# Performance work log

Hardware: AMD Instinct MI355X
Metric: run time of the kernel (lower is better)

## Reference

```python
import jax, jax.numpy as jnp
import numpy as np

B, S, D, H = 2, 2048, 1024, 16
DK = D // H

def setup_inputs() -> dict:
    key = jax.random.key(0)
    ks = jax.random.split(key, 12)
    scale = 1.0 / np.sqrt(D)
    return {
        "q": jax.random.normal(ks[0], (B, S, D), jnp.float32),
        "k": jax.random.normal(ks[1], (B, S, D), jnp.float32),
        "v": jax.random.normal(ks[2], (B, S, D), jnp.float32),
        "mask": jax.random.randint(ks[3], (B, 1, S, S), 0, 2, jnp.int32),
        "w_q": jax.random.normal(ks[4], (D, D), jnp.float32) * scale,
        "b_q": jnp.zeros((D,), jnp.float32),
        "w_k": jax.random.normal(ks[5], (D, D), jnp.float32) * scale,
        "b_k": jnp.zeros((D,), jnp.float32),
        "w_v": jax.random.normal(ks[6], (D, D), jnp.float32) * scale,
        "b_v": jnp.zeros((D,), jnp.float32),
        "w_o": jax.random.normal(ks[7], (D, D), jnp.float32) * scale,
        "b_o": jnp.zeros((D,), jnp.float32),
    }

def reference(q, k, v, mask, w_q, b_q, w_k, b_k, w_v, b_v, w_o, b_o):
    # projections (nn.Linear: x @ W^T + b)
    Q = q @ w_q.T + b_q  # [B,S,D]
    K = k @ w_k.T + b_k
    V = v @ w_v.T + b_v
    # split heads -> [B,H,S,DK]
    Q = Q.reshape(B, S, H, DK).transpose(0, 2, 1, 3)
    K = K.reshape(B, S, H, DK).transpose(0, 2, 1, 3)
    V = V.reshape(B, S, H, DK).transpose(0, 2, 1, 3)
    scores = jnp.einsum("bhqd,bhkd->bhqk", Q, K) / jnp.sqrt(jnp.float32(DK))
    scores = jnp.where(mask == 0, jnp.float32(-1e9), scores)
    attn = jax.nn.softmax(scores, axis=-1)  # dropout p=0 -> identity
    x = jnp.einsum("bhqk,bhkd->bhqd", attn, V)
    x = x.transpose(0, 2, 1, 3).reshape(B, S, D)
    return x @ w_o.T + b_o
```

## Files before the change

### kernel.cpp

```cpp
#include <hip/hip_runtime.h>
#include <hip/hip_bf16.h>
#include <cstdint>
#include <cstddef>

typedef short bf16x8 __attribute__((ext_vector_type(8)));
typedef short bf16x4v __attribute__((ext_vector_type(4)));
typedef float f32x4 __attribute__((ext_vector_type(4)));
typedef unsigned int uint32x2 __attribute__((ext_vector_type(2)));
typedef __hip_bfloat16 bf16;

constexpr int Bb = 2, Ss = 2048, Dd = 1024, Hh = 16, DKk = 64;

__device__ __forceinline__ void async_lds16(void* lds, const void* g) {
  __builtin_amdgcn_global_load_lds(
      (const __attribute__((address_space(1))) void*)g,
      (__attribute__((address_space(3))) void*)lds, 16, 0, 0);
}

__device__ __forceinline__ float bf2f(bf16 x) { return __bfloat162float(x); }
__device__ __forceinline__ short f2bf(float x) {
  bf16 h = __float2bfloat16(x);
  return *(short*)&h;
}
__device__ __forceinline__ short f2bf_fast(float x) {
  return (short)((__float_as_uint(x) + 0x8000u) >> 16);
}
__device__ __forceinline__ float bfs2f(short s) {
  return __uint_as_float(((uint32_t)(uint16_t)s) << 16);
}
__device__ __forceinline__ uint32_t cvtpk_bf16(float lo, float hi) {
  uint32_t r;
  asm("v_cvt_pk_bf16_f32 %0, %1, %2" : "=v"(r) : "v"(lo), "v"(hi));
  return r;
}
__device__ __forceinline__ uint32x2 pl32swap(uint32_t d, uint32_t s) {
  return __builtin_amdgcn_permlane32_swap(d, s, false, false);
}
__device__ __forceinline__ uint32x2 pl16swap(uint32_t d, uint32_t s) {
  return __builtin_amdgcn_permlane16_swap(d, s, false, false);
}

struct CvtArgs {
  const float* src[12];
  short* dst[12];
  int n[12];
  int count;
};

__global__ __launch_bounds__(256)
void cvt_all(CvtArgs a, const int* __restrict__ mask, uint32_t* __restrict__ bits)
{
  const int t = blockIdx.y;
  if (t == 11) {
    const int stride = 1024 * 256;
    int i = blockIdx.x * 256 + threadIdx.x;
#pragma unroll 4
    for (int it = 0; it < 32; ++it, i += stride) {
      const unsigned long long bal = __ballot(mask[i] != 0);
      if ((threadIdx.x & 63) == 0)
        *(unsigned long long*)(bits + (i >> 5)) = bal;
    }
    return;
  }
  if (t >= a.count) return;
  const float* s = a.src[t];
  short* d = a.dst[t];
  const int n = a.n[t];
  const int stride = gridDim.x * blockDim.x * 4;
  for (int i = (blockIdx.x * blockDim.x + threadIdx.x) * 4; i < n; i += stride) {
    const float4 v = *(const float4*)(s + i);
    bf16x4v o;
    o[0] = f2bf(v.x); o[1] = f2bf(v.y); o[2] = f2bf(v.z); o[3] = f2bf(v.w);
    *(bf16x4v*)(d + i) = o;
  }
}

__global__ __launch_bounds__(256, 3)
void gemm_bt(const bf16* __restrict__ A0, const bf16* __restrict__ A1, const bf16* __restrict__ A2,
             const bf16* __restrict__ W0, const bf16* __restrict__ W1, const bf16* __restrict__ W2,
             const bf16* __restrict__ b0, const bf16* __restrict__ b1, const bf16* __restrict__ b2,
             void* __restrict__ O0, void* __restrict__ O1, void* __restrict__ O2,
             float scale0, int vtrans)
{
  extern __shared__ char smem[];
  const int mt  = blockIdx.x;
  const int by  = blockIdx.y;
  const int mat = by >> 3;
  const int nt  = by & 7;
  const bf16* A    = (mat == 0) ? A0 : (mat == 1) ? A1 : A2;
  const bf16* W    = (mat == 0) ? W0 : (mat == 1) ? W1 : W2;
  const bf16* bias = (mat == 0) ? b0 : (mat == 1) ? b1 : b2;
  void*       Out  = (mat == 0) ? O0 : (mat == 1) ? O1 : O2;
  const float scale = (mat == 0) ? scale0 : 1.0f;

  const int tid  = threadIdx.x;
  const int w    = tid >> 6;
  const int lane = tid & 63;
  const int quad = lane >> 4;
  const int l16  = lane & 15;
  const int wm   = (w & 1) * 64;
  const int wn   = (w >> 1) * 64;

  const int srow = lane >> 3;
  const int sseg = (lane & 7) ^ srow;

  const char* Abytes = (const char*)A;
  const char* Wbytes = (const char*)W;

  f32x4 acc[4][4];
#pragma unroll
  for (int i = 0; i < 4; ++i)
#pragma unroll
    for (int j = 0; j < 4; ++j) acc[i][j] = f32x4{0.f, 0.f, 0.f, 0.f};

  for (int kt = 0; kt < 16; ++kt) {
    __syncthreads();
#pragma unroll
    for (int c = 0; c < 4; ++c) {
      const int r0 = w * 32 + c * 8;
      async_lds16(smem + r0 * 128,
                  Abytes + (size_t)(mt * 128 + r0 + srow) * 2048 + kt * 128 + sseg * 16);
      async_lds16(smem + 16384 + r0 * 128,
                  Wbytes + (size_t)(nt * 128 + r0 + srow) * 2048 + kt * 128 + sseg * 16);
    }
    __syncthreads();
#pragma unroll
    for (int s = 0; s < 2; ++s) {
      bf16x8 af[4], bfg[4];
#pragma unroll
      for (int mb = 0; mb < 4; ++mb) {
        const int row = wm + mb * 16 + l16;
        af[mb] = *(const bf16x8*)(smem + row * 128 + (((4 * s + quad) ^ (row & 7)) * 16));
      }
#pragma unroll
      for (int nb = 0; nb < 4; ++nb) {
        const int row = wn + nb * 16 + l16;
        bfg[nb] = *(const bf16x8*)(smem + 16384 + row * 128 + (((4 * s + quad) ^ (row & 7)) * 16));
      }
#pragma unroll
      for (int mb = 0; mb < 4; ++mb)
#pragma unroll
        for (int nb = 0; nb < 4; ++nb)
          acc[mb][nb] = __builtin_amdgcn_mfma_f32_16x16x32_bf16(af[mb], bfg[nb], acc[mb][nb], 0, 0, 0);
    }
  }

  if (vtrans && mat == 2) {
    __syncthreads();
#pragma unroll
    for (int nb = 0; nb < 4; ++nb) {
      const int dk = wn + nb * 16 + l16;
      const float bv = bf2f(bias[nt * 128 + dk]);
#pragma unroll
      for (int mb = 0; mb < 4; ++mb) {
        const int s0 = wm + mb * 16 + quad * 4;
        bf16x4v pk;
#pragma unroll
        for (int r = 0; r < 4; ++r) pk[r] = f2bf_fast(acc[mb][nb][r] + bv);
        *(bf16x4v*)(smem + dk * 256 + (((s0 >> 3) ^ (dk & 15)) * 16) + (s0 & 7) * 2) = pk;
      }
    }
    __syncthreads();
    const int bidx  = (mt * 128) >> 11;
    const int sbase = (mt * 128) & 2047;
#pragma unroll
    for (int i = 0; i < 8; ++i) {
      const int dk  = i * 16 + (tid >> 4);
      const int seg = tid & 15;
      bf16x8 vrow = *(const bf16x8*)(smem + dk * 256 + ((seg ^ (dk & 15)) * 16));
      *(bf16x8*)((bf16*)Out + (size_t)bidx * 2097152 + (size_t)(nt * 128 + dk) * 2048
                 + sbase + seg * 8) = vrow;
    }
  } else {
#pragma unroll
    for (int nb = 0; nb < 4; ++nb) {
      const int col = nt * 128 + wn + nb * 16 + l16;
      const float bv = bf2f(bias[col]);
#pragma unroll
      for (int mb = 0; mb < 4; ++mb) {
#pragma unroll
        for (int r = 0; r < 4; ++r) {
          const int row = mt * 128 + wm + mb * 16 + quad * 4 + r;
          short s = f2bf_fast((acc[mb][nb][r] + bv) * scale);
          ((short*)Out)[(size_t)row * 1024 + col] = s;
        }
      }
    }
  }
}

__global__ __launch_bounds__(256, 4)
void gemm_out(const bf16* __restrict__ A, const bf16* __restrict__ W,
              const bf16* __restrict__ bias, float* __restrict__ Out)
{
  __shared__ char smem[16384];
  const int mt = blockIdx.x;
  const int nt = blockIdx.y;
  const int tid = threadIdx.x, w = tid >> 6, lane = tid & 63;
  const int quad = lane >> 4, l16 = lane & 15;
  const int wm = (w & 1) * 32, wn = (w >> 1) * 32;
  const int srow = lane >> 3;
  const int sseg = (lane & 7) ^ (srow & 7);

  const char* Abytes = (const char*)A;
  const char* Wbytes = (const char*)W;

  f32x4 acc[2][2];
#pragma unroll
  for (int i = 0; i < 2; ++i)
#pragma unroll
    for (int j = 0; j < 2; ++j) acc[i][j] = f32x4{0.f, 0.f, 0.f, 0.f};

  for (int kt = 0; kt < 16; ++kt) {
    __syncthreads();
#pragma unroll
    for (int c = 0; c < 2; ++c) {
      const int r0 = c * 32 + w * 8;
      async_lds16(smem + c * 4096 + w * 1024,
                  Abytes + (size_t)(mt * 64 + r0 + srow) * 2048 + kt * 128 + sseg * 16);
      async_lds16(smem + 8192 + c * 4096 + w * 1024,
                  Wbytes + (size_t)(nt * 64 + r0 + srow) * 2048 + kt * 128 + sseg * 16);
    }
    __syncthreads();
#pragma unroll
    for (int s = 0; s < 2; ++s) {
      bf16x8 af[2], bfg[2];
#pragma unroll
      for (int mb = 0; mb < 2; ++mb) {
        const int row = wm + mb * 16 + l16;
        af[mb] = *(const bf16x8*)(smem + row * 128 + (((4 * s + quad) ^ (row & 7)) * 16));
      }
#pragma unroll
      for (int nb = 0; nb < 2; ++nb) {
        const int row = wn + nb * 16 + l16;
        bfg[nb] = *(const bf16x8*)(smem + 8192 + row * 128 + (((4 * s + quad) ^ (row & 7)) * 16));
      }
#pragma unroll
      for (int mb = 0; mb < 2; ++mb)
#pragma unroll
        for (int nb = 0; nb < 2; ++nb)
          acc[mb][nb] = __builtin_amdgcn_mfma_f32_16x16x32_bf16(af[mb], bfg[nb], acc[mb][nb], 0, 0, 0);
    }
  }

#pragma unroll
  for (int nb = 0; nb < 2; ++nb) {
    const int col = nt * 64 + wn + nb * 16 + l16;
    const float bv = bf2f(bias[col]);
#pragma unroll
    for (int mb = 0; mb < 2; ++mb) {
#pragma unroll
      for (int r = 0; r < 4; ++r) {
        const int row = mt * 64 + wm + mb * 16 + quad * 4 + r;
        Out[(size_t)row * 1024 + col] = acc[mb][nb][r] + bv;
      }
    }
  }
}

__device__ __forceinline__ void stage_kv(char* KbB, char* VtB,
    const bf16* __restrict__ Kp, const bf16* __restrict__ VpT,
    size_t headoff, size_t vbase, int kb, int w, int lane)
{
#pragma unroll
  for (int c = 0; c < 4; ++c) {
    const int rowK = c * 32 + w * 8 + (lane >> 3);
    const int segK = (lane & 7) ^ (rowK & 7);
    async_lds16(KbB + c * 4096 + w * 1024,
                Kp + headoff + (size_t)(kb + rowK) * Dd + segK * 8);
    const int rowV = c * 16 + w * 4 + (lane >> 4);
    const int segV = (lane & 15) ^ (rowV & 15);
    async_lds16(VtB + c * 4096 + w * 1024,
                VpT + vbase + (size_t)rowV * 2048 + kb + segV * 8);
  }
}

__global__ __launch_bounds__(256, 2)
void attn(const bf16* __restrict__ Qp, const bf16* __restrict__ Kp,
          const bf16* __restrict__ VpT, const uint32_t* __restrict__ mbits,
          bf16* __restrict__ Opart, float* __restrict__ Lpart)
{
  __shared__ char smem[65536];

  const int tile  = blockIdx.x;
  const int split = blockIdx.y;
  const int qt = tile & 15, h = (tile >> 4) & 15, b = tile >> 8;
  const int tid = threadIdx.x, w = tid >> 6, lane = tid & 63;
  const int quad = lane >> 4, l16 = lane & 15;
  const int qb = qt * 128;
  const size_t headoff = (size_t)b * (Ss * Dd) + h * DKk;
  const size_t vbase = (size_t)b * 2097152 + (size_t)h * 131072;

  const int kc0 = split * 8;
  const int kc1 = kc0 + 8;

  bf16x8 qf[2][2];
#pragma unroll
  for (int set = 0; set < 2; ++set)
#pragma unroll
    for (int s2 = 0; s2 < 2; ++s2) {
      const int row = qb + w * 32 + set * 16 + l16;
      qf[set][s2] = *(const bf16x8*)(Qp + headoff + (size_t)row * Dd + s2 * 32 + quad * 8);
    }

  bf16x8 onesv;
#pragma unroll
  for (int j = 0; j < 8; ++j) onesv[j] = (short)0x3F80;

  f32x4 o[2][4];
  f32x4 oL[2];
#pragma unroll
  for (int set = 0; set < 2; ++set) {
    oL[set] = f32x4{0.f, 0.f, 0.f, 0.f};
#pragma unroll
    for (int nbk = 0; nbk < 4; ++nbk) o[set][nbk] = f32x4{0.f, 0.f, 0.f, 0.f};
  }

  const uint32_t* mrow0 = mbits + (size_t)(b * Ss + qb + w * 32 + l16) * 64;
  const uint32_t* mrow1 = mrow0 + 16 * 64;

  char* KbC = smem;
  char* VtC = smem + 16384;
  char* KbN = smem + 32768;
  char* VtN = smem + 49152;

  uint4 mc0v = *(const uint4*)(mrow0 + kc0 * 4);
  uint4 mc1v = *(const uint4*)(mrow1 + kc0 * 4);
  stage_kv(KbC, VtC, Kp, VpT, headoff, vbase, kc0 * 128, w, lane);

  for (int kc = kc0; kc < kc1; ++kc) {
    uint4 mn0v = mc0v, mn1v = mc1v;
    if (kc + 1 < kc1) {
      mn0v = *(const uint4*)(mrow0 + (kc + 1) * 4);
      mn1v = *(const uint4*)(mrow1 + (kc + 1) * 4);
      stage_kv(KbN, VtN, Kp, VpT, headoff, vbase, (kc + 1) * 128, w, lane);
      asm volatile("s_waitcnt vmcnt(8)" ::: "memory");
    } else {
      asm volatile("s_waitcnt vmcnt(0)" ::: "memory");
    }
    __builtin_amdgcn_s_barrier();
    __builtin_amdgcn_sched_barrier(0);

    const uint32_t mc0a[4] = {mc0v.x, mc0v.y, mc0v.z, mc0v.w};
    const uint32_t mc1a[4] = {mc1v.x, mc1v.y, mc1v.z, mc1v.w};

#pragma unroll
    for (int sl = 0; sl < 4; ++sl) {
      f32x4 sc[2][2];
#pragma unroll
      for (int set = 0; set < 2; ++set)
#pragma unroll
        for (int nbh = 0; nbh < 2; ++nbh) sc[set][nbh] = f32x4{0.f, 0.f, 0.f, 0.f};
      __builtin_amdgcn_s_setprio(1);
#pragma unroll
      for (int s2 = 0; s2 < 2; ++s2)
#pragma unroll
        for (int nbh = 0; nbh < 2; ++nbh) {
          const int row = (sl * 2 + nbh) * 16 + l16;
          bf16x8 kf = *(const bf16x8*)(KbC + row * 128 + (((s2 * 4 + quad) ^ (row & 7)) * 16));
          sc[0][nbh] = __builtin_amdgcn_mfma_f32_16x16x32_bf16(kf, qf[0][s2], sc[0][nbh], 0, 0, 0);
          sc[1][nbh] = __builtin_amdgcn_mfma_f32_16x16x32_bf16(kf, qf[1][s2], sc[1][nbh], 0, 0, 0);
        }
      __builtin_amdgcn_s_setprio(0);

      bf16x8 pf[2];
#pragma unroll
      for (int set = 0; set < 2; ++set) {
        const uint32_t mword = (set == 0) ? mc0a[sl] : mc1a[sl];
        uint32_t pk[2][2];
#pragma unroll
        for (int nbh = 0; nbh < 2; ++nbh) {
          const uint32_t nib = (mword >> (nbh * 16 + quad * 4)) & 0xFu;
          const float e0 = __builtin_amdgcn_exp2f(sc[set][nbh][0]);
          const float e1 = __builtin_amdgcn_exp2f(sc[set][nbh][1]);
          const float e2 = __builtin_amdgcn_exp2f(sc[set][nbh][2]);
          const float e3 = __builtin_amdgcn_exp2f(sc[set][nbh][3]);
          const float p0 = (nib & 1u) ? e0 : 0.f;
          const float p1 = (nib & 2u) ? e1 : 0.f;
          const float p2 = (nib & 4u) ? e2 : 0.f;
          const float p3 = (nib & 8u) ? e3 : 0.f;
          pk[nbh][0] = cvtpk_bf16(p0, p1);
          pk[nbh][1] = cvtpk_bf16(p2, p3);
        }
        const uint32x2 r0 = pl32swap(pk[0][0], pk[1][0]);
        const uint32x2 r1 = pl32swap(pk[0][1], pk[1][1]);
        const uint32x2 t0 = pl16swap(r0.x, r0.y);
        const uint32x2 t1 = pl16swap(r1.x, r1.y);
        union { uint32_t u[4]; bf16x8 v; } U;
        U.u[0] = t0.x; U.u[1] = t1.x; U.u[2] = t0.y; U.u[3] = t1.y;
        pf[set] = U.v;
      }

      __builtin_amdgcn_s_setprio(1);
      oL[0] = __builtin_amdgcn_mfma_f32_16x16x32_bf16(pf[0], onesv, oL[0], 0, 0, 0);
      oL[1] = __builtin_amdgcn_mfma_f32_16x16x32_bf16(pf[1], onesv, oL[1], 0, 0, 0);
#pragma unroll
      for (int nbk = 0; nbk < 4; ++nbk) {
        const int row = nbk * 16 + l16;
        bf16x8 vf = *(const bf16x8*)(VtC + row * 256 + (((sl * 4 + quad) ^ (row & 15)) * 16));
        o[0][nbk] = __builtin_amdgcn_mfma_f32_16x16x32_bf16(pf[0], vf, o[0][nbk], 0, 0, 0);
        o[1][nbk] = __builtin_amdgcn_mfma_f32_16x16x32_bf16(pf[1], vf, o[1][nbk], 0, 0, 0);
      }
      __builtin_amdgcn_s_setprio(0);
    }

    asm volatile("" ::: "memory");
    __builtin_amdgcn_s_barrier();

    char* tp;
    tp = KbC; KbC = KbN; KbN = tp;
    tp = VtC; VtC = VtN; VtN = tp;
    mc0v = mn0v; mc1v = mn1v;
  }

#pragma unroll
  for (int set = 0; set < 2; ++set) {
    const int rbase = tile * 128 + w * 32 + set * 16;
#pragma unroll
    for (int r = 0; r < 4; ++r) {
      const int rglob = rbase + quad * 4 + r;
#pragma unroll
      for (int nbk = 0; nbk < 4; ++nbk) {
        short s = f2bf_fast(o[set][nbk][r]);
        ((short*)Opart)[((size_t)split * 65536 + rglob) * 64 + nbk * 16 + l16] = s;
      }
    }
    if (l16 == 0) {
#pragma unroll
      for (int r = 0; r < 4; ++r)
        Lpart[(size_t)split * 65536 + rbase + quad * 4 + r] = oL[set][r];
    }
  }
}

__global__ __launch_bounds__(256)
void combine(const bf16* __restrict__ Opart, const float* __restrict__ Lpart,
             bf16* __restrict__ Xa)
{
  const int t = threadIdx.x;
  const int row = blockIdx.x * 32 + (t >> 3);
  const int dkc = (t & 7) * 8;
  const float L = Lpart[row] + Lpart[65536 + row];
  const float inv = 1.0f / L;
  const bf16x8 O0 = *(const bf16x8*)(Opart + (size_t)row * 64 + dkc);
  const bf16x8 O1 = *(const bf16x8*)(Opart + ((size_t)65536 + row) * 64 + dkc);
  bf16x8 res;
#pragma unroll
  for (int j = 0; j < 8; ++j)
    res[j] = f2bf_fast((bfs2f(O0[j]) + bfs2f(O1[j])) * inv);
  const int tile = row >> 7, qlocal = row & 127;
  const int b = tile >> 8, h = (tile >> 4) & 15, q = (tile & 15) * 128 + qlocal;
  *(bf16x8*)(Xa + (size_t)(b * 2048 + q) * 1024 + h * 64 + dkc) = res;
}

extern "C" void kernel_launch(void* const* d_in, const int* in_sizes, int n_in,
                              void* d_out, int out_size, void* d_ws, size_t ws_size,
                              hipStream_t stream)
{
  const float* q  = (const float*)d_in[0];
  const float* k  = (const float*)d_in[1];
  const float* v  = (const float*)d_in[2];
  const int*   mk = (const int*)d_in[3];
  const float* wq = (const float*)d_in[4];
  const float* bq = (const float*)d_in[5];
  const float* wk = (const float*)d_in[6];
  const float* bk = (const float*)d_in[7];
  const float* wv = (const float*)d_in[8];
  const float* bv = (const float*)d_in[9];
  const float* wo = (const float*)d_in[10];
  const float* bo = (const float*)d_in[11];
  float* out = (float*)d_out;

  char* ws = (char*)d_ws;
  bf16* qb_  = (bf16*)(ws + ((size_t)0  << 20));
  bf16* kb_  = (bf16*)(ws + ((size_t)8  << 20));
  bf16* vb_  = (bf16*)(ws + ((size_t)16 << 20));
  bf16* Qp   = (bf16*)(ws + ((size_t)24 << 20));
  bf16* Kp   = (bf16*)(ws + ((size_t)32 << 20));
  bf16* VpT  = (bf16*)(ws + ((size_t)40 << 20));
  bf16* wqb  = (bf16*)(ws + ((size_t)48 << 20));
  bf16* wkb  = (bf16*)(ws + ((size_t)50 << 20));
  bf16* wvb  = (bf16*)(ws + ((size_t)52 << 20));
  bf16* wob  = (bf16*)(ws + ((size_t)54 << 20));
  bf16* bqb  = (bf16*)(ws + ((size_t)56 << 20));
  bf16* bkb  = (bf16*)(ws + ((size_t)56 << 20) + 2048);
  bf16* bvb  = (bf16*)(ws + ((size_t)56 << 20) + 4096);
  bf16* bob  = (bf16*)(ws + ((size_t)56 << 20) + 6144);
  uint32_t* mbits = (uint32_t*)(ws + ((size_t)56 << 20) + 65536);
  bf16*  Opart = (bf16*)(ws + ((size_t)0 << 20));
  float* Lpart = (float*)(ws + ((size_t)48 << 20));
  bf16*  Xa    = (bf16*)(ws + ((size_t)24 << 20));

  const int NA = Bb * Ss * Dd;
  const int NW = Dd * Dd;

  CvtArgs ca;
  ca.src[0] = q;  ca.dst[0] = (short*)qb_; ca.n[0] = NA;
  ca.src[1] = k;  ca.dst[1] = (short*)kb_; ca.n[1] = NA;
  ca.src[2] = v;  ca.dst[2] = (short*)vb_; ca.n[2] = NA;
  ca.src[3] = wq; ca.dst[3] = (short*)wqb; ca.n[3] = NW;
  ca.src[4] = wk; ca.dst[4] = (short*)wkb; ca.n[4] = NW;
  ca.src[5] = wv; ca.dst[5] = (short*)wvb; ca.n[5] = NW;
  ca.src[6] = wo; ca.dst[6] = (short*)wob; ca.n[6] = NW;
  ca.src[7] = bq; ca.dst[7] = (short*)bqb; ca.n[7] = Dd;
  ca.src[8] = bk; ca.dst[8] = (short*)bkb; ca.n[8] = Dd;
  ca.src[9] = bv; ca.dst[9] = (short*)bvb; ca.n[9] = Dd;
  ca.src[10] = bo; ca.dst[10] = (short*)bob; ca.n[10] = Dd;
  ca.src[11] = bo; ca.dst[11] = (short*)bob; ca.n[11] = 0;
  ca.count = 11;

  dim3 blk(256);
  cvt_all<<<dim3(1024, 12), blk, 0, stream>>>(ca, mk, mbits);

  gemm_bt<<<dim3(32, 24), blk, 32768, stream>>>(qb_, kb_, vb_, wqb, wkb, wvb,
                                                bqb, bkb, bvb,
                                                (void*)Qp, (void*)Kp, (void*)VpT,
                                                0.125f * 1.44269504088896340736f, 1);
  attn<<<dim3(512, 2), blk, 0, stream>>>(Qp, Kp, VpT, mbits, Opart, Lpart);
  combine<<<dim3(2048), blk, 0, stream>>>(Opart, Lpart, Xa);
  gemm_out<<<dim3(64, 16), blk, 0, stream>>>(Xa, wob, bob, out);
}
```

Measured before the change: 254.9 us.

## Drop K/V double buffering to halve LDS and raise occupancy

Replaces the double-buffered K/V LDS staging with a single 32 KB buffer that is loaded and then synchronized each iteration. The launch-bounds hint is raised to allow four blocks per CU. The aim is to hide memory latency through more resident waves rather than explicit software prefetch. In exchange, loads no longer overlap compute within a block. The tighter register budget from the higher occupancy hint may cause spills.

```diff
diff --git a/kernel.cpp b/kernel.cpp
--- a/kernel.cpp
+++ b/kernel.cpp
@@ -275,12 +275,14 @@
   }
 }
 
-__global__ __launch_bounds__(256, 2)
+__global__ __launch_bounds__(256, 4)
 void attn(const bf16* __restrict__ Qp, const bf16* __restrict__ Kp,
           const bf16* __restrict__ VpT, const uint32_t* __restrict__ mbits,
           bf16* __restrict__ Opart, float* __restrict__ Lpart)
 {
-  __shared__ char smem[65536];
+  __shared__ char smem[32768];
+  char* Kb = smem;
+  char* Vt = smem + 16384;
 
   const int tile  = blockIdx.x;
   const int split = blockIdx.y;
@@ -319,30 +321,16 @@
   const uint32_t* mrow0 = mbits + (size_t)(b * Ss + qb + w * 32 + l16) * 64;
   const uint32_t* mrow1 = mrow0 + 16 * 64;
 
-  char* KbC = smem;
-  char* VtC = smem + 16384;
-  char* KbN = smem + 32768;
-  char* VtN = smem + 49152;
-
-  uint4 mc0v = *(const uint4*)(mrow0 + kc0 * 4);
-  uint4 mc1v = *(const uint4*)(mrow1 + kc0 * 4);
-  stage_kv(KbC, VtC, Kp, VpT, headoff, vbase, kc0 * 128, w, lane);
-
   for (int kc = kc0; kc < kc1; ++kc) {
-    uint4 mn0v = mc0v, mn1v = mc1v;
-    if (kc + 1 < kc1) {
-      mn0v = *(const uint4*)(mrow0 + (kc + 1) * 4);
-      mn1v = *(const uint4*)(mrow1 + (kc + 1) * 4);
-      stage_kv(KbN, VtN, Kp, VpT, headoff, vbase, (kc + 1) * 128, w, lane);
-      asm volatile("s_waitcnt vmcnt(8)" ::: "memory");
-    } else {
-      asm volatile("s_waitcnt vmcnt(0)" ::: "memory");
-    }
-    __builtin_amdgcn_s_barrier();
-    __builtin_amdgcn_sched_barrier(0);
-
-    const uint32_t mc0a[4] = {mc0v.x, mc0v.y, mc0v.z, mc0v.w};
-    const uint32_t mc1a[4] = {mc1v.x, mc1v.y, mc1v.z, mc1v.w};
+    const int kb = kc * 128;
+    const uint4 mwv0 = *(const uint4*)(mrow0 + kc * 4);
+    const uint4 mwv1 = *(const uint4*)(mrow1 + kc * 4);
+    __syncthreads();
+    stage_kv(Kb, Vt, Kp, VpT, headoff, vbase, kb, w, lane);
+    __syncthreads();
+
+    const uint32_t mw0[4] = {mwv0.x, mwv0.y, mwv0.z, mwv0.w};
+    const uint32_t mw1[4] = {mwv1.x, mwv1.y, mwv1.z, mwv1.w};
 
 #pragma unroll
     for (int sl = 0; sl < 4; ++sl) {
@@ -357,7 +345,7 @@
 #pragma unroll
         for (int nbh = 0; nbh < 2; ++nbh) {
           const int row = (sl * 2 + nbh) * 16 + l16;
-          bf16x8 kf = *(const bf16x8*)(KbC + row * 128 + (((s2 * 4 + quad) ^ (row & 7)) * 16));
+          bf16x8 kf = *(const bf16x8*)(Kb + row * 128 + (((s2 * 4 + quad) ^ (row & 7)) * 16));
           sc[0][nbh] = __builtin_amdgcn_mfma_f32_16x16x32_bf16(kf, qf[0][s2], sc[0][nbh], 0, 0, 0);
           sc[1][nbh] = __builtin_amdgcn_mfma_f32_16x16x32_bf16(kf, qf[1][s2], sc[1][nbh], 0, 0, 0);
         }
@@ -366,7 +354,7 @@
       bf16x8 pf[2];
 #pragma unroll
       for (int set = 0; set < 2; ++set) {
-        const uint32_t mword = (set == 0) ? mc0a[sl] : mc1a[sl];
+        const uint32_t mword = (set == 0) ? mw0[sl] : mw1[sl];
         uint32_t pk[2][2];
 #pragma unroll
         for (int nbh = 0; nbh < 2; ++nbh) {
@@ -397,20 +385,12 @@
 #pragma unroll
       for (int nbk = 0; nbk < 4; ++nbk) {
         const int row = nbk * 16 + l16;
-        bf16x8 vf = *(const bf16x8*)(VtC + row * 256 + (((sl * 4 + quad) ^ (row & 15)) * 16));
+        bf16x8 vf = *(const bf16x8*)(Vt + row * 256 + (((sl * 4 + quad) ^ (row & 15)) * 16));
         o[0][nbk] = __builtin_amdgcn_mfma_f32_16x16x32_bf16(pf[0], vf, o[0][nbk], 0, 0, 0);
         o[1][nbk] = __builtin_amdgcn_mfma_f32_16x16x32_bf16(pf[1], vf, o[1][nbk], 0, 0, 0);
       }
       __builtin_amdgcn_s_setprio(0);
     }
-
-    asm volatile("" ::: "memory");
-    __builtin_amdgcn_s_barrier();
-
-    char* tp;
-    tp = KbC; KbC = KbN; KbN = tp;
-    tp = VtC; VtC = VtN; VtN = tp;
-    mc0v = mn0v; mc1v = mn1v;
   }
 
 #pragma unroll
```

After: 260.9 us. +2.4%, slower.
